# Performance work log

Hardware: AMD Instinct MI355X
Metric: run time of the kernel (lower is better)

## Reference

```python
import jax, jax.numpy as jnp
import numpy as np

K = 4  # spline order (degree K-1)


def bspline_basis(x, t, k):
    """Evaluate the k nonzero B-spline basis functions of order k at x.

    x: [B, I] floats; t: [G+2k-1] clamped knot vector.
    Returns (idx [B,I,k] int32 basis indices, basis [B,I,k] values),
    using the de Boor / NURBS-book triangular recursion (vectorized over B,I;
    Python loops only over the small fixed order k).
    """
    m = t.shape[0]
    # interval index: t[i] <= x < t[i+1], clamped to valid span [k-1, m-k-1]
    i = jnp.clip(jnp.searchsorted(t, x, side='right') - 1, k - 1, m - k - 1)
    p = k - 1
    N = [jnp.ones_like(x)]
    left, right = [], []
    for j in range(1, p + 1):
        left.append(x - t[i + 1 - j])
        right.append(t[i + j] - x)
        saved = jnp.zeros_like(x)
        Nn = []
        for r in range(j):
            temp = N[r] / (right[r] + left[j - 1 - r])
            Nn.append(saved + right[r] * temp)
            saved = left[j - 1 - r] * temp
        Nn.append(saved)
        N = Nn
    idx = jnp.stack([i - p + j for j in range(k)], axis=-1)   # [B,I,k]
    basis = jnp.stack(N, axis=-1)                             # [B,I,k]
    return idx, basis


def setup_inputs() -> dict:
    key = jax.random.key(0)
    k1, k2 = jax.random.split(key)
    B, I, O, G, k = 2048, 128, 128, 64, K
    t0, t1 = -1.0, 1.0
    x = jax.random.uniform(k1, (B, I), jnp.float32, minval=t0, maxval=t1)
    # xavier_normal_ for fan_in=in_dim, fan_out=out_dim (per-slice heuristic)
    std = (2.0 / (I + O)) ** 0.5
    w = jax.random.normal(k2, (G + k, I, O), jnp.float32) * std
    t = jnp.concatenate([
        jnp.full((k - 1,), t0, jnp.float32),
        jnp.linspace(t0, t1, G + 1, dtype=jnp.float32),
        jnp.full((k - 1,), t1, jnp.float32),
    ])
    return {"x": x, "w": w, "t": t}


def reference(x, w, t):
    k = K
    B, I = x.shape
    O = w.shape[2]
    idx, basis = bspline_basis(x, t, k)                       # [B,I,k]
    # activation slot uses the last row of w (torch index -1)
    act_idx = jnp.full((B, I, 1), w.shape[0] - 1, idx.dtype)
    idx_full = jnp.concatenate([idx, act_idx], axis=-1)       # [B,I,k+1]
    y = jnp.concatenate([basis, jax.nn.silu(x)[..., None]], axis=-1)  # [B,I,k+1]
    wt = jnp.transpose(w, (1, 0, 2))                          # [I, G+k, O]
    w2 = wt[jnp.arange(I)[None, :, None], idx_full]           # [B,I,k+1,O] gather
    return jnp.einsum('bij,bijo->bo', y, w2)                  # [B,O]
```

## Files before the change

kernel.cpp:

```cpp
#include <hip/hip_runtime.h>
#include <math.h>

#define B_TOTAL 2048
#define I_DIM   128
#define O_DIM   128
#define GK      68
#define NKNOT   71
#define W_ELEMS ((size_t)GK * I_DIM * O_DIM)
#define WS_MIN  (W_ELEMS * 2)

__device__ __forceinline__ float rdlanef(float v, int l) {
    return __int_as_float(__builtin_amdgcn_readlane(__float_as_int(v), l));
}
__device__ __forceinline__ unsigned short f2bf(float f) {
    unsigned u = __float_as_uint(f);
    return (unsigned short)((u + 0x7fffu + ((u >> 16) & 1u)) >> 16);
}
__device__ __forceinline__ float bflo(unsigned u) { return __uint_as_float(u << 16); }
__device__ __forceinline__ float bfhi(unsigned u) { return __uint_as_float(u & 0xffff0000u); }

__global__ __launch_bounds__(256)
void wcvt(const float* __restrict__ w, unsigned short* __restrict__ wbf) {
    const int tid = threadIdx.x;
    const int p   = blockIdx.x * 8 + (tid >> 5);
    const int oq  = (tid & 31) * 4;
    const int g   = p >> 7;
    const int i   = p & 127;
    const float4 v = *(const float4*)(w + (size_t)p * O_DIM + oq);
    ushort4 o4;
    o4.x = f2bf(v.x); o4.y = f2bf(v.y); o4.z = f2bf(v.z); o4.w = f2bf(v.w);
    *(ushort4*)(wbf + ((size_t)i * GK + g) * O_DIM + oq) = o4;
}

__global__ __launch_bounds__(256, 8)
void flashkan_gather(const float* __restrict__ x,
                     const unsigned short* __restrict__ wbf,
                     const float* __restrict__ t,
                     float* __restrict__ out) {
    __shared__ float t_sh[NKNOT];
    __shared__ float psum[4][O_DIM];

    const int tid  = threadIdx.x;
    const int b    = blockIdx.x;
    const int wave = tid >> 6;
    const int lane = tid & 63;
    const int l32  = lane & 31;

    if (tid < NKNOT) t_sh[tid] = t[tid];
    __syncthreads();

    float cf0, cf1, cf2, cf3, cf4;
    int   cg;
    {
        const float xv = x[(size_t)b * I_DIM + wave * 32 + l32];

        int ik = 3 + (int)floorf((xv + 1.0f) * 32.0f);
        ik = min(max(ik, 3), 66);
        while (ik < 66 && xv >= t_sh[ik + 1]) ++ik;
        while (ik > 3 && xv < t_sh[ik]) --ik;

        float l0, l1, l2, r0, r1, r2;
        float N0 = 1.0f, N1, N2, N3;
        l0 = xv - t_sh[ik];
        r0 = t_sh[ik + 1] - xv;
        {
            float temp = N0 / (r0 + l0);
            N0 = r0 * temp;
            N1 = l0 * temp;
        }
        l1 = xv - t_sh[ik - 1];
        r1 = t_sh[ik + 2] - xv;
        {
            float saved = 0.0f, temp;
            temp = N0 / (r0 + l1);
            N0 = saved + r0 * temp;
            saved = l1 * temp;
            temp = N1 / (r1 + l0);
            N1 = saved + r1 * temp;
            N2 = l0 * temp;
        }
        l2 = xv - t_sh[ik - 2];
        r2 = t_sh[ik + 3] - xv;
        {
            float saved = 0.0f, temp;
            temp = N0 / (r0 + l2);
            N0 = saved + r0 * temp;
            saved = l2 * temp;
            temp = N1 / (r1 + l1);
            N1 = saved + r1 * temp;
            saved = l1 * temp;
            temp = N2 / (r2 + l0);
            N2 = saved + r2 * temp;
            N3 = l0 * temp;
        }
        cf0 = N0; cf1 = N1; cf2 = N2; cf3 = N3;
        cf4 = xv / (1.0f + expf(-xv));
        cg  = ik - 3;
    }

    const int i_base = wave * 32;
    float ax = 0.0f, ay = 0.0f;

    #pragma unroll
    for (int k = 0; k < 32; ++k) {
        const float c0 = rdlanef(cf0, k);
        const float c1 = rdlanef(cf1, k);
        const float c2 = rdlanef(cf2, k);
        const float c3 = rdlanef(cf3, k);
        const float c4 = rdlanef(cf4, k);
        const int   g0 = __builtin_amdgcn_readlane(cg, k);

        const int i = i_base + k;
        const unsigned* rp = (const unsigned*)(wbf + (((size_t)i * GK + g0) << 7)) + lane;
        const unsigned* sp = (const unsigned*)(wbf + (((size_t)i * GK + 67) << 7)) + lane;
        const unsigned u0 = rp[0];
        const unsigned u1 = rp[64];
        const unsigned u2 = rp[128];
        const unsigned u3 = rp[192];
        const unsigned u4 = *sp;

        ax += c0 * bflo(u0) + c1 * bflo(u1) + c2 * bflo(u2)
            + c3 * bflo(u3) + c4 * bflo(u4);
        ay += c0 * bfhi(u0) + c1 * bfhi(u1) + c2 * bfhi(u2)
            + c3 * bfhi(u3) + c4 * bfhi(u4);
    }

    psum[wave][lane * 2]     = ax;
    psum[wave][lane * 2 + 1] = ay;
    __syncthreads();

    if (tid < O_DIM) {
        out[(size_t)b * O_DIM + tid] =
            psum[0][tid] + psum[1][tid] + psum[2][tid] + psum[3][tid];
    }
}

__global__ __launch_bounds__(256)
void flashkan_gather_f32(const float* __restrict__ x,
                         const float* __restrict__ w,
                         const float* __restrict__ t,
                         float* __restrict__ out) {
    __shared__ float t_sh[NKNOT];
    __shared__ float psum[4][O_DIM];

    const int tid  = threadIdx.x;
    const int b    = blockIdx.x;
    const int wave = tid >> 6;
    const int lane = tid & 63;
    const int l32  = lane & 31;

    if (tid < NKNOT) t_sh[tid] = t[tid];
    __syncthreads();

    float cf0, cf1, cf2, cf3, cf4;
    int   cg;
    {
        const float xv = x[(size_t)b * I_DIM + wave * 32 + l32];
        int ik = 3 + (int)floorf((xv + 1.0f) * 32.0f);
        ik = min(max(ik, 3), 66);
        while (ik < 66 && xv >= t_sh[ik + 1]) ++ik;
        while (ik > 3 && xv < t_sh[ik]) --ik;
        float l0, l1, l2, r0, r1, r2;
        float N0 = 1.0f, N1, N2, N3;
        l0 = xv - t_sh[ik];  r0 = t_sh[ik + 1] - xv;
        { float temp = N0 / (r0 + l0); N0 = r0 * temp; N1 = l0 * temp; }
        l1 = xv - t_sh[ik - 1];  r1 = t_sh[ik + 2] - xv;
        { float saved = 0.0f, temp;
          temp = N0 / (r0 + l1); N0 = saved + r0 * temp; saved = l1 * temp;
          temp = N1 / (r1 + l0); N1 = saved + r1 * temp; N2 = l0 * temp; }
        l2 = xv - t_sh[ik - 2];  r2 = t_sh[ik + 3] - xv;
        { float saved = 0.0f, temp;
          temp = N0 / (r0 + l2); N0 = saved + r0 * temp; saved = l2 * temp;
          temp = N1 / (r1 + l1); N1 = saved + r1 * temp; saved = l1 * temp;
          temp = N2 / (r2 + l0); N2 = saved + r2 * temp; N3 = l0 * temp; }
        cf0 = N0; cf1 = N1; cf2 = N2; cf3 = N3;
        cf4 = xv / (1.0f + expf(-xv));
        cg  = ik - 3;
    }

    const int i_base = wave * 32;
    float ax = 0.0f, ay = 0.0f;
    #pragma unroll 8
    for (int k = 0; k < 32; ++k) {
        const float c0 = rdlanef(cf0, k);
        const float c1 = rdlanef(cf1, k);
        const float c2 = rdlanef(cf2, k);
        const float c3 = rdlanef(cf3, k);
        const float c4 = rdlanef(cf4, k);
        const int   g0 = __builtin_amdgcn_readlane(cg, k);
        const int i = i_base + k;
        const float2* base = (const float2*)(w + (size_t)i * O_DIM) + lane;
        const size_t rs = (size_t)I_DIM * O_DIM / 2;
        const float2 v0 = base[(size_t)g0 * rs];
        const float2 v1 = base[(size_t)(g0 + 1) * rs];
        const float2 v2 = base[(size_t)(g0 + 2) * rs];
        const float2 v3 = base[(size_t)(g0 + 3) * rs];
        const float2 v4 = base[(size_t)(GK - 1) * rs];
        ax += c0 * v0.x + c1 * v1.x + c2 * v2.x + c3 * v3.x + c4 * v4.x;
        ay += c0 * v0.y + c1 * v1.y + c2 * v2.y + c3 * v3.y + c4 * v4.y;
    }

    psum[wave][lane * 2]     = ax;
    psum[wave][lane * 2 + 1] = ay;
    __syncthreads();
    if (tid < O_DIM) {
        out[(size_t)b * O_DIM + tid] =
            psum[0][tid] + psum[1][tid] + psum[2][tid] + psum[3][tid];
    }
}

extern "C" void kernel_launch(void* const* d_in, const int* in_sizes, int n_in,
                              void* d_out, int out_size, void* d_ws, size_t ws_size,
                              hipStream_t stream) {
    const float* x = (const float*)d_in[0];
    const float* w = (const float*)d_in[1];
    const float* t = (const float*)d_in[2];
    float* out = (float*)d_out;

    if (ws_size >= WS_MIN) {
        unsigned short* wbf = (unsigned short*)d_ws;
        wcvt<<<(int)(W_ELEMS / (8 * 128)), 256, 0, stream>>>(w, wbf);
        flashkan_gather<<<B_TOTAL, 256, 0, stream>>>(x, wbf, t, out);
    } else {
        flashkan_gather_f32<<<B_TOTAL, 256, 0, stream>>>(x, w, t, out);
    }
}
```

Baseline: 30.95 us.

## Replace per-row gather kernel with bf16 MFMA dense-K GEMM and split-I reduction

```diff
diff --git a/kernel.cpp b/kernel.cpp
--- a/kernel.cpp
+++ b/kernel.cpp
@@ -6,135 +6,204 @@
 #define O_DIM   128
 #define GK      68
 #define NKNOT   71
-#define W_ELEMS ((size_t)GK * I_DIM * O_DIM)
-#define WS_MIN  (W_ELEMS * 2)
-
-__device__ __forceinline__ float rdlanef(float v, int l) {
-    return __int_as_float(__builtin_amdgcn_readlane(__float_as_int(v), l));
-}
+#define NT      8
+#define KS      3
+#define FRAGS   (NT * KS)
+#define SLICE_US (FRAGS * 512)
+#define BT      128
+#define BTILES  (B_TOTAL / BT)
+#define RI      8
+#define NR      (I_DIM / RI)
+#define PART_FLOATS ((size_t)NR * B_TOTAL * O_DIM)
+#define WFRAG_OFF   (PART_FLOATS * 4)
+#define WFRAG_BYTES ((size_t)I_DIM * SLICE_US * 2)
+#define WS_NEED     (WFRAG_OFF + WFRAG_BYTES)
+
+typedef short  s16x8 __attribute__((ext_vector_type(8)));
+typedef float  f32x4 __attribute__((ext_vector_type(4)));
+
 __device__ __forceinline__ unsigned short f2bf(float f) {
     unsigned u = __float_as_uint(f);
     return (unsigned short)((u + 0x7fffu + ((u >> 16) & 1u)) >> 16);
 }
-__device__ __forceinline__ float bflo(unsigned u) { return __uint_as_float(u << 16); }
-__device__ __forceinline__ float bfhi(unsigned u) { return __uint_as_float(u & 0xffff0000u); }
+
+struct Coef { unsigned short h0, h1, h2, h3, h4; int g0; };
+
+__device__ __forceinline__ Coef coef_eval(const float* __restrict__ x,
+                                          const float* t_sh, int b, int i) {
+    const float xv = x[(size_t)b * I_DIM + i];
+    int ik = 3 + (int)floorf((xv + 1.0f) * 32.0f);
+    ik = min(max(ik, 3), 66);
+    while (ik < 66 && xv >= t_sh[ik + 1]) ++ik;
+    while (ik > 3 && xv < t_sh[ik]) --ik;
+    float l0, l1, l2, r0, r1, r2;
+    float N0 = 1.0f, N1, N2, N3;
+    l0 = xv - t_sh[ik];  r0 = t_sh[ik + 1] - xv;
+    { float temp = N0 / (r0 + l0); N0 = r0 * temp; N1 = l0 * temp; }
+    l1 = xv - t_sh[ik - 1];  r1 = t_sh[ik + 2] - xv;
+    { float saved = 0.0f, temp;
+      temp = N0 / (r0 + l1); N0 = saved + r0 * temp; saved = l1 * temp;
+      temp = N1 / (r1 + l0); N1 = saved + r1 * temp; N2 = l0 * temp; }
+    l2 = xv - t_sh[ik - 2];  r2 = t_sh[ik + 3] - xv;
+    { float saved = 0.0f, temp;
+      temp = N0 / (r0 + l2); N0 = saved + r0 * temp; saved = l2 * temp;
+      temp = N1 / (r1 + l1); N1 = saved + r1 * temp; saved = l1 * temp;
+      temp = N2 / (r2 + l0); N2 = saved + r2 * temp; N3 = l0 * temp; }
+    const float silu = xv / (1.0f + expf(-xv));
+    Coef c;
+    c.h0 = f2bf(N0); c.h1 = f2bf(N1); c.h2 = f2bf(N2); c.h3 = f2bf(N3);
+    c.h4 = f2bf(silu);
+    c.g0 = ik - 3;
+    return c;
+}
 
 __global__ __launch_bounds__(256)
-void wcvt(const float* __restrict__ w, unsigned short* __restrict__ wbf) {
-    const int tid = threadIdx.x;
-    const int p   = blockIdx.x * 8 + (tid >> 5);
-    const int oq  = (tid & 31) * 4;
-    const int g   = p >> 7;
-    const int i   = p & 127;
-    const float4 v = *(const float4*)(w + (size_t)p * O_DIM + oq);
-    ushort4 o4;
-    o4.x = f2bf(v.x); o4.y = f2bf(v.y); o4.z = f2bf(v.z); o4.w = f2bf(v.w);
-    *(ushort4*)(wbf + ((size_t)i * GK + g) * O_DIM + oq) = o4;
-}
-
-__global__ __launch_bounds__(256, 8)
-void flashkan_gather(const float* __restrict__ x,
-                     const unsigned short* __restrict__ wbf,
-                     const float* __restrict__ t,
-                     float* __restrict__ out) {
+void wcvt(const float* __restrict__ w, unsigned short* __restrict__ wf) {
+    const int bid  = blockIdx.x;
+    const int i    = bid / 6;
+    const int wave = threadIdx.x >> 6;
+    const int lane = threadIdx.x & 63;
+    const int f    = (bid % 6) * 4 + wave;
+    const int nt   = f / 3;
+    const int ks   = f % 3;
+    const int o    = nt * 16 + (lane & 15);
+    const int kb   = ks * 32 + ((lane >> 4) << 3);
+
+    unsigned short v[8];
+    #pragma unroll
+    for (int j = 0; j < 8; ++j) {
+        const int k = kb + j;
+        float s = 0.0f;
+        if (k < GK) s = w[(size_t)k * (I_DIM * O_DIM) + (size_t)i * O_DIM + o];
+        v[j] = f2bf(s);
+    }
+    uint4 st;
+    st.x = (unsigned)v[0] | ((unsigned)v[1] << 16);
+    st.y = (unsigned)v[2] | ((unsigned)v[3] << 16);
+    st.z = (unsigned)v[4] | ((unsigned)v[5] << 16);
+    st.w = (unsigned)v[6] | ((unsigned)v[7] << 16);
+    *(uint4*)(wf + (size_t)i * SLICE_US + f * 512 + lane * 8) = st;
+}
+
+__global__ __launch_bounds__(512, 2)
+void flashkan_mfma(const float* __restrict__ x,
+                   const unsigned short* __restrict__ wf,
+                   const float* __restrict__ t,
+                   float* __restrict__ part) {
+    __shared__ __align__(16) unsigned short sbuf[2][SLICE_US];
     __shared__ float t_sh[NKNOT];
-    __shared__ float psum[4][O_DIM];
 
     const int tid  = threadIdx.x;
-    const int b    = blockIdx.x;
-    const int wave = tid >> 6;
-    const int lane = tid & 63;
-    const int l32  = lane & 31;
+    const int bid  = blockIdx.x;
+    const int btile = bid >> 4;
+    const int ir    = bid & 15;
+    const int b0    = btile * BT;
+    const int i0    = ir * RI;
+    const int wave  = tid >> 6;
+    const int lane  = tid & 63;
+    const int wm    = wave >> 1;
+    const int wn    = wave & 1;
+    const int rowA  = b0 + wm * 32 + (lane & 15);
+    const int rowB  = rowA + 16;
+    const int k0g   = (lane >> 4) << 3;
 
     if (tid < NKNOT) t_sh[tid] = t[tid];
     __syncthreads();
 
-    float cf0, cf1, cf2, cf3, cf4;
-    int   cg;
-    {
-        const float xv = x[(size_t)b * I_DIM + wave * 32 + l32];
-
-        int ik = 3 + (int)floorf((xv + 1.0f) * 32.0f);
-        ik = min(max(ik, 3), 66);
-        while (ik < 66 && xv >= t_sh[ik + 1]) ++ik;
-        while (ik > 3 && xv < t_sh[ik]) --ik;
-
-        float l0, l1, l2, r0, r1, r2;
-        float N0 = 1.0f, N1, N2, N3;
-        l0 = xv - t_sh[ik];
-        r0 = t_sh[ik + 1] - xv;
-        {
-            float temp = N0 / (r0 + l0);
-            N0 = r0 * temp;
-            N1 = l0 * temp;
-        }
-        l1 = xv - t_sh[ik - 1];
-        r1 = t_sh[ik + 2] - xv;
-        {
-            float saved = 0.0f, temp;
-            temp = N0 / (r0 + l1);
-            N0 = saved + r0 * temp;
-            saved = l1 * temp;
-            temp = N1 / (r1 + l0);
-            N1 = saved + r1 * temp;
-            N2 = l0 * temp;
-        }
-        l2 = xv - t_sh[ik - 2];
-        r2 = t_sh[ik + 3] - xv;
-        {
-            float saved = 0.0f, temp;
-            temp = N0 / (r0 + l2);
-            N0 = saved + r0 * temp;
-            saved = l2 * temp;
-            temp = N1 / (r1 + l1);
-            N1 = saved + r1 * temp;
-            saved = l1 * temp;
-            temp = N2 / (r2 + l0);
-            N2 = saved + r2 * temp;
-            N3 = l0 * temp;
-        }
-        cf0 = N0; cf1 = N1; cf2 = N2; cf3 = N3;
-        cf4 = xv / (1.0f + expf(-xv));
-        cg  = ik - 3;
-    }
-
-    const int i_base = wave * 32;
-    float ax = 0.0f, ay = 0.0f;
-
-    #pragma unroll
-    for (int k = 0; k < 32; ++k) {
-        const float c0 = rdlanef(cf0, k);
-        const float c1 = rdlanef(cf1, k);
-        const float c2 = rdlanef(cf2, k);
-        const float c3 = rdlanef(cf3, k);
-        const float c4 = rdlanef(cf4, k);
-        const int   g0 = __builtin_amdgcn_readlane(cg, k);
-
-        const int i = i_base + k;
-        const unsigned* rp = (const unsigned*)(wbf + (((size_t)i * GK + g0) << 7)) + lane;
-        const unsigned* sp = (const unsigned*)(wbf + (((size_t)i * GK + 67) << 7)) + lane;
-        const unsigned u0 = rp[0];
-        const unsigned u1 = rp[64];
-        const unsigned u2 = rp[128];
-        const unsigned u3 = rp[192];
-        const unsigned u4 = *sp;
-
-        ax += c0 * bflo(u0) + c1 * bflo(u1) + c2 * bflo(u2)
-            + c3 * bflo(u3) + c4 * bflo(u4);
-        ay += c0 * bfhi(u0) + c1 * bfhi(u1) + c2 * bfhi(u2)
-            + c3 * bfhi(u3) + c4 * bfhi(u4);
-    }
-
-    psum[wave][lane * 2]     = ax;
-    psum[wave][lane * 2 + 1] = ay;
-    __syncthreads();
-
-    if (tid < O_DIM) {
-        out[(size_t)b * O_DIM + tid] =
-            psum[0][tid] + psum[1][tid] + psum[2][tid] + psum[3][tid];
-    }
-}
-
+    auto stage = [&](int sel, int i_abs) {
+        #pragma unroll
+        for (int q = 0; q < 3; ++q) {
+            const int c = q * 8 + wave;
+            const unsigned short* src = wf + (size_t)i_abs * SLICE_US + c * 512 + lane * 8;
+            void* dstp = (void*)((char*)&sbuf[sel][0] + c * 1024);
+            __builtin_amdgcn_global_load_lds(
+                (const __attribute__((address_space(1))) void*)src,
+                (__attribute__((address_space(3))) void*)dstp,
+                16, 0, 0);
+        }
+    };
+
+    f32x4 accA[4], accB[4];
+    #pragma unroll
+    for (int n = 0; n < 4; ++n) { accA[n] = (f32x4)0.0f; accB[n] = (f32x4)0.0f; }
+
+    auto build_a = [&](const Coef& c, int ks) -> s16x8 {
+        const int k0 = ks * 32 + k0g;
+        s16x8 a;
+        #pragma unroll
+        for (int j = 0; j < 8; ++j) {
+            const int dk = k0 + j - c.g0;
+            const int k  = k0 + j;
+            unsigned short v = 0;
+            v = (dk == 0) ? c.h0 : v;
+            v = (dk == 1) ? c.h1 : v;
+            v = (dk == 2) ? c.h2 : v;
+            v = (dk == 3) ? c.h3 : v;
+            v = (k == 67) ? c.h4 : v;
+            a[j] = (short)v;
+        }
+        return a;
+    };
+
+    auto compute = [&](int i_abs, const unsigned short* buf) {
+        const Coef cA = coef_eval(x, t_sh, rowA, i_abs);
+        const Coef cB = coef_eval(x, t_sh, rowB, i_abs);
+        #pragma unroll
+        for (int ks = 0; ks < KS; ++ks) {
+            const s16x8 aA = build_a(cA, ks);
+            const s16x8 aB = build_a(cB, ks);
+            #pragma unroll
+            for (int n = 0; n < 4; ++n) {
+                const int nt = wn * 4 + n;
+                const s16x8 bf = *(const s16x8*)((const char*)buf +
+                                   ((nt * 3 + ks) << 10) + (lane << 4));
+                accA[n] = __builtin_amdgcn_mfma_f32_16x16x32_bf16(aA, bf, accA[n], 0, 0, 0);
+                accB[n] = __builtin_amdgcn_mfma_f32_16x16x32_bf16(aB, bf, accB[n], 0, 0, 0);
+            }
+        }
+    };
+
+    stage(0, i0);
+    __syncthreads();
+
+    for (int ii = 0; ii < RI; ii += 2) {
+        stage(1, i0 + ii + 1);
+        compute(i0 + ii, sbuf[0]);
+        __syncthreads();
+        if (ii + 2 < RI) stage(0, i0 + ii + 2);
+        compute(i0 + ii + 1, sbuf[1]);
+        __syncthreads();
+    }
+
+    float* pbase = part + (size_t)ir * (B_TOTAL * O_DIM);
+    #pragma unroll
+    for (int n = 0; n < 4; ++n) {
+        const int o = (wn * 4 + n) * 16 + (lane & 15);
+        #pragma unroll
+        for (int r = 0; r < 4; ++r) {
+            const int bA = b0 + wm * 32 + (lane >> 4) * 4 + r;
+            pbase[(size_t)bA * O_DIM + o]        = accA[n][r];
+            pbase[(size_t)(bA + 16) * O_DIM + o] = accB[n][r];
+        }
+    }
+}
+
+__global__ __launch_bounds__(256)
+void flashkan_reduce(const float* __restrict__ ws, float* __restrict__ out) {
+    const int f = blockIdx.x * 256 + threadIdx.x;
+    const float4* base = (const float4*)ws + f;
+    float4 s = make_float4(0.0f, 0.0f, 0.0f, 0.0f);
+    #pragma unroll
+    for (int r2 = 0; r2 < NR; ++r2) {
+        const float4 v = base[(size_t)r2 * (B_TOTAL * O_DIM / 4)];
+        s.x += v.x; s.y += v.y; s.z += v.z; s.w += v.w;
+    }
+    ((float4*)out)[f] = s;
+}
+
+__device__ __forceinline__ float rdlanef(float v, int l) {
+    return __int_as_float(__builtin_amdgcn_readlane(__float_as_int(v), l));
+}
 __global__ __launch_bounds__(256)
 void flashkan_gather_f32(const float* __restrict__ x,
                          const float* __restrict__ w,
@@ -142,18 +211,14 @@
                          float* __restrict__ out) {
     __shared__ float t_sh[NKNOT];
     __shared__ float psum[4][O_DIM];
-
     const int tid  = threadIdx.x;
     const int b    = blockIdx.x;
     const int wave = tid >> 6;
     const int lane = tid & 63;
     const int l32  = lane & 31;
-
     if (tid < NKNOT) t_sh[tid] = t[tid];
     __syncthreads();
-
-    float cf0, cf1, cf2, cf3, cf4;
-    int   cg;
+    float cf0, cf1, cf2, cf3, cf4; int cg;
     {
         const float xv = x[(size_t)b * I_DIM + wave * 32 + l32];
         int ik = 3 + (int)floorf((xv + 1.0f) * 32.0f);
@@ -177,15 +242,12 @@
         cf4 = xv / (1.0f + expf(-xv));
         cg  = ik - 3;
     }
-
     const int i_base = wave * 32;
     float ax = 0.0f, ay = 0.0f;
     #pragma unroll 8
     for (int k = 0; k < 32; ++k) {
-        const float c0 = rdlanef(cf0, k);
-        const float c1 = rdlanef(cf1, k);
-        const float c2 = rdlanef(cf2, k);
-        const float c3 = rdlanef(cf3, k);
+        const float c0 = rdlanef(cf0, k), c1 = rdlanef(cf1, k);
+        const float c2 = rdlanef(cf2, k), c3 = rdlanef(cf3, k);
         const float c4 = rdlanef(cf4, k);
         const int   g0 = __builtin_amdgcn_readlane(cg, k);
         const int i = i_base + k;
@@ -199,7 +261,6 @@
         ax += c0 * v0.x + c1 * v1.x + c2 * v2.x + c3 * v3.x + c4 * v4.x;
         ay += c0 * v0.y + c1 * v1.y + c2 * v2.y + c3 * v3.y + c4 * v4.y;
     }
-
     psum[wave][lane * 2]     = ax;
     psum[wave][lane * 2 + 1] = ay;
     __syncthreads();
@@ -217,10 +278,12 @@
     const float* t = (const float*)d_in[2];
     float* out = (float*)d_out;
 
-    if (ws_size >= WS_MIN) {
-        unsigned short* wbf = (unsigned short*)d_ws;
-        wcvt<<<(int)(W_ELEMS / (8 * 128)), 256, 0, stream>>>(w, wbf);
-        flashkan_gather<<<B_TOTAL, 256, 0, stream>>>(x, wbf, t, out);
+    if (ws_size >= WS_NEED) {
+        float* part = (float*)d_ws;
+        unsigned short* wfr = (unsigned short*)((char*)d_ws + WFRAG_OFF);
+        wcvt<<<I_DIM * 6, 256, 0, stream>>>(w, wfr);
+        flashkan_mfma<<<BTILES * NR, 512, 0, stream>>>(x, wfr, t, part);
+        flashkan_reduce<<<B_TOTAL * O_DIM / 4 / 256, 256, 0, stream>>>(part, out);
     } else {
         flashkan_gather_f32<<<B_TOTAL, 256, 0, stream>>>(x, w, t, out);
     }
```

Result: slower. 57.06 us (+84.4%).
